# Kernel tuning notes

Hardware: AMD Instinct MI355X
Metric: run time of the kernel (lower is better)

## Reference

```python
import jax, jax.numpy as jnp
import numpy as np
from jax.ops import segment_sum

NUM_NODES = 50000
IN_DIM = 512
OUT_DIM = 512
NNZ = 150000
NUM_EDGES = 10000


def setup_inputs() -> dict:
    key = jax.random.key(0)
    k1, k2, k3, k4, k5 = jax.random.split(key, 5)
    X = jax.random.normal(k1, (NUM_NODES, IN_DIM), dtype=jnp.float32)
    V = jax.random.randint(k2, (NNZ,), 0, NUM_NODES)
    E = jax.random.randint(k3, (NNZ,), 0, NUM_EDGES)
    # Linear(in_dim, out_dim) params (torch default init ~ U(-1/sqrt(in), 1/sqrt(in)))
    bound = 1.0 / np.sqrt(IN_DIM)
    W = jax.random.uniform(k4, (OUT_DIM, IN_DIM), minval=-bound, maxval=bound, dtype=jnp.float32)
    b = jax.random.uniform(k5, (OUT_DIM,), minval=-bound, maxval=bound, dtype=jnp.float32)
    eps = jnp.float32(0.1)
    return {"X": X, "V": V, "E": E, "num_edges": NUM_EDGES, "W": W, "b": b, "eps": eps}


def reference(X, V, E, num_edges, W, b, eps):
    num_nodes = X.shape[0]
    # Stage 1: node -> hyperedge (mean of member node features)
    gathered = X[V]  # (nnz, in_dim)
    edge_sum = segment_sum(gathered, E, num_segments=num_edges)          # (num_edges, in_dim)
    count = segment_sum(jnp.ones((E.shape[0],), X.dtype), E, num_segments=num_edges)
    edge_emb = edge_sum / jnp.clip(count, 1.0)[:, None]
    # Stage 2: hyperedge -> node (sum of incident hyperedge embeddings)
    node_msg = segment_sum(edge_emb[E], V, num_segments=num_nodes)       # (num_nodes, in_dim)
    # GIN self-loop + linear
    h = (1.0 + eps) * X + node_msg
    return h @ W.T + b
```

## Files before the change

kernel.cpp:

```cpp
#include <hip/hip_runtime.h>

#define D     512
#define NEDGE 10000
#define ECAP  64
#define NCAP  32

typedef __attribute__((ext_vector_type(8))) short  bf16x8;
typedef __attribute__((ext_vector_type(4))) float  f32x4;
typedef __attribute__((ext_vector_type(8))) unsigned short u16x8;

static __device__ __forceinline__ unsigned short f2bf(float f) {
    union { float f; unsigned u; } c; c.f = f;
    unsigned u = c.u;
    return (unsigned short)((u + 0x7FFFu + ((u >> 16) & 1u)) >> 16);
}
static __device__ __forceinline__ float bf2f(unsigned short s) {
    union { unsigned u; float f; } c; c.u = ((unsigned)s) << 16; return c.f;
}

__global__ __launch_bounds__(256)
void prep(const int* __restrict__ V, const int* __restrict__ E,
          const float* __restrict__ W, const float* __restrict__ X,
          int* __restrict__ ecnt, int* __restrict__ ncnt,
          int* __restrict__ emem, int* __restrict__ nmem,
          unsigned short* __restrict__ wb, unsigned short* __restrict__ xb,
          int nnz, int xgroups)
{
    const int i = blockIdx.x * 256 + threadIdx.x;
    if (i < nnz) {
        const int e = E[i], v = V[i];
        const int p = atomicAdd(&ecnt[e], 1);
        if (p < ECAP) emem[e * ECAP + p] = v;
        const int q = atomicAdd(&ncnt[v], 1);
        if (q < NCAP) nmem[v * NCAP + q] = e;
    }
    if (i < xgroups) {
        const float4 a = *(reinterpret_cast<const float4*>(X) + (size_t)i * 2);
        const float4 b = *(reinterpret_cast<const float4*>(X) + (size_t)i * 2 + 1);
        u16x8 o;
        o[0] = f2bf(a.x); o[1] = f2bf(a.y); o[2] = f2bf(a.z); o[3] = f2bf(a.w);
        o[4] = f2bf(b.x); o[5] = f2bf(b.y); o[6] = f2bf(b.z); o[7] = f2bf(b.w);
        *(reinterpret_cast<u16x8*>(xb) + i) = o;
    }
    if (i < D * D / 8) {
        const float4 a = *(reinterpret_cast<const float4*>(W) + (size_t)i * 2);
        const float4 b = *(reinterpret_cast<const float4*>(W) + (size_t)i * 2 + 1);
        u16x8 o;
        o[0] = f2bf(a.x); o[1] = f2bf(a.y); o[2] = f2bf(a.z); o[3] = f2bf(a.w);
        o[4] = f2bf(b.x); o[5] = f2bf(b.y); o[6] = f2bf(b.z); o[7] = f2bf(b.w);
        *(reinterpret_cast<u16x8*>(wb) + i) = o;
    }
}

__global__ __launch_bounds__(256)
void edge_gather(const unsigned short* __restrict__ xb, const int* __restrict__ ecnt,
                 const int* __restrict__ emem, unsigned short* __restrict__ edge_emb)
{
    __shared__ float red[D];
    const int e = blockIdx.x;
    const int t = threadIdx.x;
    const int half = t >> 7;
    const int l = t & 127;
    int deg = ecnt[e]; if (deg > ECAP) deg = ECAP;
    const int* lst = emem + e * ECAP;
    float4 acc = make_float4(0.f, 0.f, 0.f, 0.f);
    for (int m = half; m < deg; m += 2) {
        const int v = lst[m];
        const ushort4 x = *reinterpret_cast<const ushort4*>(xb + (size_t)v * D + l * 4);
        acc.x += bf2f(x.x); acc.y += bf2f(x.y);
        acc.z += bf2f(x.z); acc.w += bf2f(x.w);
    }
    if (half) *reinterpret_cast<float4*>(red + l * 4) = acc;
    __syncthreads();
    if (!half) {
        const float4 o = *reinterpret_cast<const float4*>(red + l * 4);
        const float inv = 1.0f / fmaxf((float)deg, 1.0f);
        ushort4 r;
        r.x = f2bf((acc.x + o.x) * inv);
        r.y = f2bf((acc.y + o.y) * inv);
        r.z = f2bf((acc.z + o.z) * inv);
        r.w = f2bf((acc.w + o.w) * inv);
        *reinterpret_cast<ushort4*>(edge_emb + (size_t)e * D + l * 4) = r;
    }
}

__global__ __launch_bounds__(128)
void build_h(const unsigned short* __restrict__ xb, const unsigned short* __restrict__ edge_emb,
             const int* __restrict__ ncnt, const int* __restrict__ nmem,
             const float* __restrict__ eps_p, unsigned short* __restrict__ h, int M)
{
    const int v = blockIdx.x;
    const int t = threadIdx.x;
    float4 acc = make_float4(0.f, 0.f, 0.f, 0.f);
    if (v < M) {
        const float scale = 1.0f + *eps_p;
        const ushort4 x = *reinterpret_cast<const ushort4*>(xb + (size_t)v * D + t * 4);
        acc.x = scale * bf2f(x.x); acc.y = scale * bf2f(x.y);
        acc.z = scale * bf2f(x.z); acc.w = scale * bf2f(x.w);
        int deg = ncnt[v]; if (deg > NCAP) deg = NCAP;
        const int* lst = nmem + v * NCAP;
        for (int m = 0; m < deg; ++m) {
            const int e = lst[m];
            const ushort4 g = *reinterpret_cast<const ushort4*>(edge_emb + (size_t)e * D + t * 4);
            acc.x += bf2f(g.x); acc.y += bf2f(g.y);
            acc.z += bf2f(g.z); acc.w += bf2f(g.w);
        }
    }
    ushort4 r;
    r.x = f2bf(acc.x); r.y = f2bf(acc.y); r.z = f2bf(acc.z); r.w = f2bf(acc.w);
    *reinterpret_cast<ushort4*>(h + (size_t)v * D + t * 4) = r;
}

__global__ __launch_bounds__(256, 5)
void gemm_bf16(const unsigned short* __restrict__ h, const unsigned short* __restrict__ wb,
               const float* __restrict__ bias, float* __restrict__ out, int M,
               int q, int r)
{
    __shared__ unsigned short As[128 * 64];
    __shared__ unsigned short Bs[128 * 64];

    const int orig = blockIdx.x;
    const int xcd = orig & 7, lin = orig >> 3;
    const int wg = (xcd < r ? xcd * (q + 1) : r * (q + 1) + (xcd - r) * q) + lin;
    const int row0 = (wg >> 2) * 128;
    const int col0 = (wg & 3) * 128;

    const int tid  = threadIdx.x;
    const int lane = tid & 63;
    const int wave = tid >> 6;
    const int wr = wave >> 1, wc = wave & 1;

    const int l15   = lane & 15;
    const int khalf = lane >> 4;
    const int crow  = lane >> 3;
    const int slot  = lane & 7;

    f32x4 acc[4][4] = {};

    for (int t = 0; t < 8; ++t) {
        const int k0 = t * 64;
        #pragma unroll
        for (int cc = 0; cc < 8; ++cc) {
            const int chunk = wave * 8 + cc;
            const unsigned short* src; unsigned short* dst; int c, base;
            if (chunk < 16) { c = chunk;      src = h;  base = row0; dst = As; }
            else            { c = chunk - 16; src = wb; base = col0; dst = Bs; }
            const int rr = c * 8 + crow;
            const int gslot = slot ^ (rr & 7);
            const unsigned short* gp = src + (size_t)(base + rr) * D + k0 + gslot * 8;
            unsigned short* lp = dst + c * 512;
            __builtin_amdgcn_global_load_lds(
                (const __attribute__((address_space(1))) void*)gp,
                (__attribute__((address_space(3))) void*)lp, 16, 0, 0);
        }
        asm volatile("s_waitcnt vmcnt(0)" ::: "memory");
        __syncthreads();

        #pragma unroll
        for (int s = 0; s < 2; ++s) {
            bf16x8 a[4], b[4];
            #pragma unroll
            for (int i = 0; i < 4; ++i) {
                const int rr = wr * 64 + i * 16 + l15;
                const int sl = (khalf | (s << 2)) ^ (rr & 7);
                a[i] = *reinterpret_cast<const bf16x8*>(As + rr * 64 + sl * 8);
            }
            #pragma unroll
            for (int j = 0; j < 4; ++j) {
                const int rr = wc * 64 + j * 16 + l15;
                const int sl = (khalf | (s << 2)) ^ (rr & 7);
                b[j] = *reinterpret_cast<const bf16x8*>(Bs + rr * 64 + sl * 8);
            }
            #pragma unroll
            for (int i = 0; i < 4; ++i)
                #pragma unroll
                for (int j = 0; j < 4; ++j)
                    acc[i][j] = __builtin_amdgcn_mfma_f32_16x16x32_bf16(a[i], b[j], acc[i][j], 0, 0, 0);
        }
        __syncthreads();
    }

    const int row4 = (lane >> 4) * 4;
    #pragma unroll
    for (int j = 0; j < 4; ++j) {
        const int gc = col0 + wc * 64 + j * 16 + l15;
        const float bv = bias[gc];
        #pragma unroll
        for (int i = 0; i < 4; ++i) {
            #pragma unroll
            for (int reg = 0; reg < 4; ++reg) {
                const int gr = row0 + wr * 64 + i * 16 + row4 + reg;
                if (gr < M) out[(size_t)gr * D + gc] = acc[i][j][reg] + bv;
            }
        }
    }
}

extern "C" void kernel_launch(void* const* d_in, const int* in_sizes, int n_in,
                              void* d_out, int out_size, void* d_ws, size_t ws_size,
                              hipStream_t stream)
{
    const float* X    = (const float*)d_in[0];
    const int*   V    = (const int*)  d_in[1];
    const int*   E    = (const int*)  d_in[2];
    const float* W    = (const float*)d_in[4];
    const float* bias = (const float*)d_in[5];
    const float* eps  = (const float*)d_in[6];
    float* out = (float*)d_out;

    const int nnz = in_sizes[1];
    const int M   = in_sizes[0] / D;
    const int Mpad = ((M + 127) / 128) * 128;

    char* w = (char*)d_ws;
    int* ecnt = (int*)w;
    int* ncnt = ecnt + 10048;
    size_t off = (10048 + 50048) * sizeof(int);
    int* emem = (int*)(w + off);            off += (size_t)NEDGE * ECAP * sizeof(int);
    int* nmem = (int*)(w + off);            off += (size_t)M * NCAP * sizeof(int);
    off = (off + 255) & ~(size_t)255;
    unsigned short* edge_emb = (unsigned short*)(w + off); off += (size_t)NEDGE * D * sizeof(unsigned short);
    unsigned short* xbuf     = (unsigned short*)(w + off); off += (size_t)M * D * sizeof(unsigned short);
    unsigned short* hbuf     = (unsigned short*)(w + off); off += (size_t)Mpad * D * sizeof(unsigned short);
    unsigned short* wbuf     = (unsigned short*)(w + off); off += (size_t)D * D * sizeof(unsigned short);

    hipMemsetAsync(ecnt, 0, (10048 + 50048) * sizeof(int), stream);

    const int xgroups = M * D / 8;
    prep<<<(xgroups + 255) / 256, 256, 0, stream>>>(V, E, W, X, ecnt, ncnt, emem, nmem,
                                                    wbuf, xbuf, nnz, xgroups);
    edge_gather<<<NEDGE, 256, 0, stream>>>(xbuf, ecnt, emem, edge_emb);
    build_h    <<<Mpad, 128, 0, stream>>>(xbuf, edge_emb, ncnt, nmem, eps, hbuf, M);

    const int nwg = (Mpad / 128) * (D / 128);
    gemm_bf16<<<nwg, 256, 0, stream>>>(hbuf, wbuf, bias, out, M, nwg / 8, nwg % 8);
}
```

Before: 176.4 us.

## Drop X bf16 conversion pass and pad adjacency atomic counters

Removes the full pass that converts X to bf16. The edge gather and build_h kernels now read fp32 X directly, so one read and one write of the whole feature matrix go away, and prep shrinks to adjacency building plus the W conversion. In exchange, the gathers move twice as many bytes per row, which relies on X staying largely cache-resident. The per-edge and per-node counters are also spaced 32 ints apart so atomics do not share cache lines, at the cost of a much larger memset.

```diff
diff --git a/kernel.cpp b/kernel.cpp
--- a/kernel.cpp
+++ b/kernel.cpp
@@ -4,6 +4,7 @@
 #define NEDGE 10000
 #define ECAP  64
 #define NCAP  32
+#define CPAD  32
 
 typedef __attribute__((ext_vector_type(8))) short  bf16x8;
 typedef __attribute__((ext_vector_type(4))) float  f32x4;
@@ -19,28 +20,19 @@
 }
 
 __global__ __launch_bounds__(256)
-void prep(const int* __restrict__ V, const int* __restrict__ E,
-          const float* __restrict__ W, const float* __restrict__ X,
-          int* __restrict__ ecnt, int* __restrict__ ncnt,
-          int* __restrict__ emem, int* __restrict__ nmem,
-          unsigned short* __restrict__ wb, unsigned short* __restrict__ xb,
-          int nnz, int xgroups)
+void adj_build(const int* __restrict__ V, const int* __restrict__ E,
+               const float* __restrict__ W,
+               int* __restrict__ ecnt, int* __restrict__ ncnt,
+               int* __restrict__ emem, int* __restrict__ nmem,
+               unsigned short* __restrict__ wb, int nnz)
 {
     const int i = blockIdx.x * 256 + threadIdx.x;
     if (i < nnz) {
         const int e = E[i], v = V[i];
-        const int p = atomicAdd(&ecnt[e], 1);
+        const int p = atomicAdd(&ecnt[(size_t)e * CPAD], 1);
         if (p < ECAP) emem[e * ECAP + p] = v;
-        const int q = atomicAdd(&ncnt[v], 1);
+        const int q = atomicAdd(&ncnt[(size_t)v * CPAD], 1);
         if (q < NCAP) nmem[v * NCAP + q] = e;
-    }
-    if (i < xgroups) {
-        const float4 a = *(reinterpret_cast<const float4*>(X) + (size_t)i * 2);
-        const float4 b = *(reinterpret_cast<const float4*>(X) + (size_t)i * 2 + 1);
-        u16x8 o;
-        o[0] = f2bf(a.x); o[1] = f2bf(a.y); o[2] = f2bf(a.z); o[3] = f2bf(a.w);
-        o[4] = f2bf(b.x); o[5] = f2bf(b.y); o[6] = f2bf(b.z); o[7] = f2bf(b.w);
-        *(reinterpret_cast<u16x8*>(xb) + i) = o;
     }
     if (i < D * D / 8) {
         const float4 a = *(reinterpret_cast<const float4*>(W) + (size_t)i * 2);
@@ -53,7 +45,7 @@
 }
 
 __global__ __launch_bounds__(256)
-void edge_gather(const unsigned short* __restrict__ xb, const int* __restrict__ ecnt,
+void edge_gather(const float* __restrict__ X, const int* __restrict__ ecnt,
                  const int* __restrict__ emem, unsigned short* __restrict__ edge_emb)
 {
     __shared__ float red[D];
@@ -61,14 +53,13 @@
     const int t = threadIdx.x;
     const int half = t >> 7;
     const int l = t & 127;
-    int deg = ecnt[e]; if (deg > ECAP) deg = ECAP;
+    int deg = ecnt[(size_t)e * CPAD]; if (deg > ECAP) deg = ECAP;
     const int* lst = emem + e * ECAP;
     float4 acc = make_float4(0.f, 0.f, 0.f, 0.f);
     for (int m = half; m < deg; m += 2) {
         const int v = lst[m];
-        const ushort4 x = *reinterpret_cast<const ushort4*>(xb + (size_t)v * D + l * 4);
-        acc.x += bf2f(x.x); acc.y += bf2f(x.y);
-        acc.z += bf2f(x.z); acc.w += bf2f(x.w);
+        const float4 x = *reinterpret_cast<const float4*>(X + (size_t)v * D + l * 4);
+        acc.x += x.x; acc.y += x.y; acc.z += x.z; acc.w += x.w;
     }
     if (half) *reinterpret_cast<float4*>(red + l * 4) = acc;
     __syncthreads();
@@ -85,7 +76,7 @@
 }
 
 __global__ __launch_bounds__(128)
-void build_h(const unsigned short* __restrict__ xb, const unsigned short* __restrict__ edge_emb,
+void build_h(const float* __restrict__ X, const unsigned short* __restrict__ edge_emb,
              const int* __restrict__ ncnt, const int* __restrict__ nmem,
              const float* __restrict__ eps_p, unsigned short* __restrict__ h, int M)
 {
@@ -94,10 +85,10 @@
     float4 acc = make_float4(0.f, 0.f, 0.f, 0.f);
     if (v < M) {
         const float scale = 1.0f + *eps_p;
-        const ushort4 x = *reinterpret_cast<const ushort4*>(xb + (size_t)v * D + t * 4);
-        acc.x = scale * bf2f(x.x); acc.y = scale * bf2f(x.y);
-        acc.z = scale * bf2f(x.z); acc.w = scale * bf2f(x.w);
-        int deg = ncnt[v]; if (deg > NCAP) deg = NCAP;
+        const float4 x = *reinterpret_cast<const float4*>(X + (size_t)v * D + t * 4);
+        acc.x = scale * x.x; acc.y = scale * x.y;
+        acc.z = scale * x.z; acc.w = scale * x.w;
+        int deg = ncnt[(size_t)v * CPAD]; if (deg > NCAP) deg = NCAP;
         const int* lst = nmem + v * NCAP;
         for (int m = 0; m < deg; ++m) {
             const int e = lst[m];
@@ -214,23 +205,21 @@
 
     char* w = (char*)d_ws;
     int* ecnt = (int*)w;
-    int* ncnt = ecnt + 10048;
-    size_t off = (10048 + 50048) * sizeof(int);
+    int* ncnt = ecnt + (size_t)NEDGE * CPAD;
+    size_t off = ((size_t)NEDGE + Mpad) * CPAD * sizeof(int);
     int* emem = (int*)(w + off);            off += (size_t)NEDGE * ECAP * sizeof(int);
     int* nmem = (int*)(w + off);            off += (size_t)M * NCAP * sizeof(int);
     off = (off + 255) & ~(size_t)255;
     unsigned short* edge_emb = (unsigned short*)(w + off); off += (size_t)NEDGE * D * sizeof(unsigned short);
-    unsigned short* xbuf     = (unsigned short*)(w + off); off += (size_t)M * D * sizeof(unsigned short);
     unsigned short* hbuf     = (unsigned short*)(w + off); off += (size_t)Mpad * D * sizeof(unsigned short);
     unsigned short* wbuf     = (unsigned short*)(w + off); off += (size_t)D * D * sizeof(unsigned short);
 
-    hipMemsetAsync(ecnt, 0, (10048 + 50048) * sizeof(int), stream);
-
-    const int xgroups = M * D / 8;
-    prep<<<(xgroups + 255) / 256, 256, 0, stream>>>(V, E, W, X, ecnt, ncnt, emem, nmem,
-                                                    wbuf, xbuf, nnz, xgroups);
-    edge_gather<<<NEDGE, 256, 0, stream>>>(xbuf, ecnt, emem, edge_emb);
-    build_h    <<<Mpad, 128, 0, stream>>>(xbuf, edge_emb, ncnt, nmem, eps, hbuf, M);
+    hipMemsetAsync(ecnt, 0, ((size_t)NEDGE + Mpad) * CPAD * sizeof(int), stream);
+
+    adj_build<<<(nnz + 255) / 256, 256, 0, stream>>>(V, E, W, ecnt, ncnt, emem, nmem,
+                                                     wbuf, nnz);
+    edge_gather<<<NEDGE, 256, 0, stream>>>(X, ecnt, emem, edge_emb);
+    build_h    <<<Mpad, 128, 0, stream>>>(X, edge_emb, ncnt, nmem, eps, hbuf, M);
 
     const int nwg = (Mpad / 128) * (D / 128);
     gemm_bf16<<<nwg, 256, 0, stream>>>(hbuf, wbuf, bias, out, M, nwg / 8, nwg % 8);
```

New measurement: 168.7 us. 1.05x faster.
